# Kernel tuning notes

Measured on AMD Instinct MI355X. Metric: run time of the kernel, lower is better.

## Reference

```python
import jax, jax.numpy as jnp
import numpy as np

B, T, D, H, HD = 128, 256, 512, 8, 64

def setup_inputs() -> dict:
    key = jax.random.key(0)
    ks = jax.random.split(key, 5)
    scale = 0.02
    return {
        "x": jax.random.normal(ks[0], (B, T, D), dtype=jnp.float32),
        "Wq": jax.random.normal(ks[1], (H, D, HD), dtype=jnp.float32) * scale,
        "Wk": jax.random.normal(ks[2], (H, D, HD), dtype=jnp.float32) * scale,
        "Wv": jax.random.normal(ks[3], (H, D, HD), dtype=jnp.float32) * scale,
        "Wo": jax.random.normal(ks[4], (D, D), dtype=jnp.float32) * scale,
        "bo": jnp.zeros((D,), dtype=jnp.float32),
    }

def reference(x, Wq, Wk, Wv, Wo, bo):
    # Per-head projections, batched over heads: [B,T,D] x [H,D,HD] -> [B,H,T,HD]
    q = jnp.einsum('btd,hdk->bhtk', x, Wq)
    k = jnp.einsum('btd,hdk->bhtk', x, Wk)
    v = jnp.einsum('btd,hdk->bhtk', x, Wv)
    # Scaled scores [B,H,T,T] with causal mask
    scores = jnp.einsum('bhtk,bhsk->bhts', q, k) * (HD ** -0.5)
    causal = jnp.tril(jnp.ones((T, T), dtype=bool))
    scores = jnp.where(causal, scores, jnp.finfo(scores.dtype).min)
    attn = jax.nn.softmax(scores, axis=-1)
    # Dropout is identity at inference.
    out = jnp.einsum('bhts,bhsk->bhtk', attn, v)
    # Concat heads: [B,T,H*HD] == [B,T,D]
    out = out.transpose(0, 2, 1, 3).reshape(B, T, D)
    # Output projection
    return out @ Wo + bo
```

## Files before the change

kernel.cpp:

```cpp
#include <hip/hip_runtime.h>
#include <hip/hip_bf16.h>

typedef __bf16 bf16x8 __attribute__((ext_vector_type(8)));
typedef __bf16 bf16x4 __attribute__((ext_vector_type(4)));
typedef float f32x4 __attribute__((ext_vector_type(4)));
typedef unsigned short u16x8 __attribute__((ext_vector_type(8)));
typedef short s16x4 __attribute__((ext_vector_type(4)));


__device__ __forceinline__ unsigned short f2bf(float f) {
  unsigned u = __float_as_uint(f);
  u += 0x7fffu + ((u >> 16) & 1u);
  return (unsigned short)(u >> 16);
}

__device__ __forceinline__ bf16x4 cvt4(f32x4 v) {
  bf16x4 o;
  o[0] = (__bf16)v[0]; o[1] = (__bf16)v[1]; o[2] = (__bf16)v[2]; o[3] = (__bf16)v[3];
  return o;
}

__device__ __forceinline__ f32x4 mfma16(bf16x4 a, bf16x4 b, f32x4 c) {
#if __has_builtin(__builtin_amdgcn_mfma_f32_16x16x16_bf16)
  return __builtin_amdgcn_mfma_f32_16x16x16_bf16(a, b, c, 0, 0, 0);
#elif __has_builtin(__builtin_amdgcn_mfma_f32_16x16x16bf16_1k)
  return __builtin_amdgcn_mfma_f32_16x16x16bf16_1k(
      __builtin_bit_cast(s16x4, a), __builtin_bit_cast(s16x4, b), c, 0, 0, 0);
#else
  f32x4 d = c;
  asm("v_mfma_f32_16x16x16_bf16 %0, %1, %2, %0" : "+v"(d) : "v"(a), "v"(b));
  return d;
#endif
}

__device__ __forceinline__ void async16(const void* g, void* l) {
  __builtin_amdgcn_global_load_lds(
      (const __attribute__((address_space(1))) void*)g,
      (__attribute__((address_space(3))) void*)l, 16, 0, 0);
}

__global__ __launch_bounds__(256) void k_convert_x(const float* __restrict__ in,
                                                   unsigned short* __restrict__ out) {
  int i = blockIdx.x * 256 + threadIdx.x;
  const float4* p = (const float4*)in + (size_t)i * 2;
  float4 a = p[0], b = p[1];
  u16x8 o;
  o[0] = f2bf(a.x); o[1] = f2bf(a.y); o[2] = f2bf(a.z); o[3] = f2bf(a.w);
  o[4] = f2bf(b.x); o[5] = f2bf(b.y); o[6] = f2bf(b.z); o[7] = f2bf(b.w);
  *((u16x8*)out + i) = o;
}

__global__ __launch_bounds__(256) void k_transpose_all(const float* __restrict__ Wq,
                                                       const float* __restrict__ Wk,
                                                       const float* __restrict__ Wv,
                                                       const float* __restrict__ Wo,
                                                       unsigned short* __restrict__ Wqkv,
                                                       unsigned short* __restrict__ Wot) {
  __shared__ unsigned short tile[64][72];
  int z = blockIdx.z;
  const float* inb;
  unsigned short* outb;
  int incols, c0;
  if (z < 3) {
    const float* w = (z == 0) ? Wq : (z == 1 ? Wk : Wv);
    inb = w + (size_t)blockIdx.x * 512 * 64;
    outb = Wqkv + ((size_t)z * 8 + blockIdx.x) * 32768;
    incols = 64; c0 = 0;
  } else {
    inb = Wo; outb = Wot; incols = 512; c0 = blockIdx.x * 64;
  }
  int r0 = blockIdx.y * 64;
  int tid = threadIdx.x;
  int r = tid >> 2, cq = (tid & 3) * 16;
  const float* src = inb + (size_t)(r0 + r) * incols + c0 + cq;
#pragma unroll
  for (int i = 0; i < 16; i += 4) {
    float4 v = *(const float4*)(src + i);
    tile[r][cq + i + 0] = f2bf(v.x);
    tile[r][cq + i + 1] = f2bf(v.y);
    tile[r][cq + i + 2] = f2bf(v.z);
    tile[r][cq + i + 3] = f2bf(v.w);
  }
  __syncthreads();
  int cr = tid >> 2, rq = (tid & 3) * 16;
  u16x8 o0, o1;
#pragma unroll
  for (int i = 0; i < 8; ++i) o0[i] = tile[rq + i][cr];
#pragma unroll
  for (int i = 0; i < 8; ++i) o1[i] = tile[rq + 8 + i][cr];
  unsigned short* dst = outb + (size_t)(c0 + cr) * 512 + r0 + rq;
  *(u16x8*)dst = o0;
  *(u16x8*)(dst + 8) = o1;
}

template <bool SWAP, int EPI>
__device__ __forceinline__ void gemm_body(
    unsigned short* smem,
    const unsigned short* __restrict__ A, const unsigned short* __restrict__ Bm,
    unsigned short* __restrict__ O0, unsigned short* __restrict__ O1,
    const float* __restrict__ bo, float* __restrict__ outf,
    int m0, int n0, int mt, bool qscale) {
  int tid = threadIdx.x, wid = tid >> 6, lane = tid & 63, lr = lane & 15, lg = lane >> 4;
  int wm = wid >> 2, wn = wid & 3;
  int arow = tid >> 2;
  int sk8 = (tid & 3) ^ ((tid >> 3) & 3);
  const unsigned short* asrc = A + (size_t)(m0 + arow) * 512 + sk8 * 8;
  const unsigned short* bsrc0 = Bm + (size_t)(n0 + arow) * 512 + sk8 * 8;
  const unsigned short* bsrc1 = Bm + (size_t)(n0 + 128 + arow) * 512 + sk8 * 8;
  int rdsw = (lg ^ ((lr >> 1) & 3)) * 8;

  f32x4 acc[4][4];
#pragma unroll
  for (int mi = 0; mi < 4; ++mi)
#pragma unroll
    for (int ni = 0; ni < 4; ++ni) acc[mi][ni] = (f32x4){0.f, 0.f, 0.f, 0.f};

#define STAGE(kb, buf)                                                   \
  {                                                                      \
    unsigned short* base_ = smem + (buf) * 12288;                        \
    async16(asrc + (kb) * 32, base_ + wid * 512);                        \
    async16(bsrc0 + (kb) * 32, base_ + 4096 + wid * 512);                \
    async16(bsrc1 + (kb) * 32, base_ + 8192 + wid * 512);                \
  }

  STAGE(0, 0)
  STAGE(1, 1)
  asm volatile("s_waitcnt vmcnt(3)" ::: "memory");
  __builtin_amdgcn_s_barrier();
  asm volatile("" ::: "memory");

#pragma unroll
  for (int t = 0; t < 16; ++t) {
    int buf = t % 3;
    bf16x8 a[4], b[4];
#pragma unroll
    for (int mi = 0; mi < 4; ++mi)
      a[mi] = *(const bf16x8*)&smem[buf * 12288 + (wm * 64 + mi * 16 + lr) * 32 + rdsw];
#pragma unroll
    for (int ni = 0; ni < 4; ++ni)
      b[ni] = *(const bf16x8*)&smem[buf * 12288 + 4096 + (wn * 64 + ni * 16 + lr) * 32 + rdsw];
    if (t < 14) STAGE(t + 2, (t + 2) % 3)
    asm volatile("" ::: "memory");
    __builtin_amdgcn_s_setprio(1);
#pragma unroll
    for (int mi = 0; mi < 4; ++mi)
#pragma unroll
      for (int ni = 0; ni < 4; ++ni) {
        if (SWAP)
          acc[mi][ni] = __builtin_amdgcn_mfma_f32_16x16x32_bf16(b[ni], a[mi], acc[mi][ni], 0, 0, 0);
        else
          acc[mi][ni] = __builtin_amdgcn_mfma_f32_16x16x32_bf16(a[mi], b[ni], acc[mi][ni], 0, 0, 0);
      }
    __builtin_amdgcn_s_setprio(0);
    if (t < 14)       asm volatile("s_waitcnt vmcnt(3)" ::: "memory");
    else if (t == 14) asm volatile("s_waitcnt vmcnt(0)" ::: "memory");
    __builtin_amdgcn_s_barrier();
    asm volatile("" ::: "memory");
  }
#undef STAGE

  int bb = mt >> 1, t0 = (mt & 1) * 128;
  if constexpr (EPI == 0) {
    if (qscale) {
#pragma unroll
      for (int mi = 0; mi < 4; ++mi)
#pragma unroll
        for (int ni = 0; ni < 4; ++ni) acc[mi][ni] *= 0.18033688011112042f;
    }
    int z = n0 >> 9;
    int h = ((n0 & 511) >> 6) + wn;
    unsigned short* outp = (z ? O1 : O0) + (size_t)(bb * 8 + h) * 16384;
#pragma unroll
    for (int ni = 0; ni < 4; ++ni) {
      int hd0 = ni * 16 + lg * 4;
#pragma unroll
      for (int mi = 0; mi < 4; ++mi) {
        int tq = t0 + wm * 64 + mi * 16 + lr;
        *(bf16x4*)&outp[(size_t)tq * 64 + hd0] = cvt4(acc[mi][ni]);
      }
    }
  } else if constexpr (EPI == 1) {
#pragma unroll
    for (int ni = 0; ni < 4; ++ni) {
      int nb = n0 + wn * 64 + ni * 16 + lg * 4;
      float4 b4 = *(const float4*)&bo[nb];
#pragma unroll
      for (int mi = 0; mi < 4; ++mi) {
        int mg = m0 + wm * 64 + mi * 16 + lr;
        float4 o;
        o.x = acc[mi][ni][0] + b4.x; o.y = acc[mi][ni][1] + b4.y;
        o.z = acc[mi][ni][2] + b4.z; o.w = acc[mi][ni][3] + b4.w;
        *(float4*)&outf[(size_t)mg * 512 + nb] = o;
      }
    }
  } else {
    int h = ((n0 & 511) >> 6) + wn;
    unsigned short* outp = O0 + (size_t)(bb * 8 + h) * 16384;
#pragma unroll
    for (int ni = 0; ni < 4; ++ni) {
      int hd = ni * 16 + lr;
#pragma unroll
      for (int mi = 0; mi < 4; ++mi) {
        int tq = t0 + wm * 64 + mi * 16 + lg * 4;
        *(bf16x4*)&outp[(size_t)hd * 256 + tq] = cvt4(acc[mi][ni]);
      }
    }
  }
}

__global__ __launch_bounds__(512, 4) void k_qkv3(
    const unsigned short* __restrict__ xb,
    const unsigned short* __restrict__ Wt,
    unsigned short* __restrict__ Qb,
    unsigned short* __restrict__ Kb,
    unsigned short* __restrict__ Vtb) {
  __shared__ unsigned short smem[36864];
  int xcd = blockIdx.x & 7, g = blockIdx.x >> 3;
  int w = xcd * 192 + g;
  int mt = w / 6, nt = w % 6;
  int m0 = mt * 128, n0 = nt * 256;
  if ((n0 >> 9) < 2)
    gemm_body<true, 0>(smem, xb, Wt, Qb, Kb, nullptr, nullptr, m0, n0, mt, n0 < 512);
  else
    gemm_body<false, 2>(smem, xb, Wt, Vtb, nullptr, nullptr, nullptr, m0, n0, mt, false);
}

__global__ __launch_bounds__(512, 4) void k_oproj(
    const unsigned short* __restrict__ Ab,
    const unsigned short* __restrict__ Wot,
    const float* __restrict__ bo,
    float* __restrict__ outf) {
  __shared__ unsigned short smem[36864];
  int xcd = blockIdx.x & 7, g = blockIdx.x >> 3;
  int w = xcd * 64 + g;
  int mt = w >> 1, nt = w & 1;
  gemm_body<true, 1>(smem, Ab, Wot, nullptr, nullptr, bo, outf, mt * 128, nt * 256, mt, false);
}

__global__ __launch_bounds__(512, 4) void k_attn2(
    const unsigned short* __restrict__ Qb,
    const unsigned short* __restrict__ Kb,
    const unsigned short* __restrict__ Vtb,
    unsigned short* __restrict__ Ob) {
  __shared__ unsigned short Ksh[256 * 72];
  __shared__ unsigned short Vsh[64 * 260];
  int bh = blockIdx.x;
  int tid = threadIdx.x, wid = tid >> 6, lane = tid & 63, lr = lane & 15, lg = lane >> 4;
  int bb = bh >> 3, h = bh & 7;
  const unsigned short* Kg = Kb + (size_t)bh * 16384;
  const unsigned short* Vg = Vtb + (size_t)bh * 16384;
  int4 gk[4], gv[4];
#pragma unroll
  for (int j = 0; j < 4; ++j) {
    int c = tid + j * 512;
    gk[j] = *(const int4*)(Kg + c * 8);
    gv[j] = *(const int4*)(Vg + c * 8);
  }
  int ci0 = wid, ci1 = 15 - wid;
  const unsigned short* q0 = Qb + (size_t)bh * 16384 + (size_t)(ci0 * 16 + lr) * 64 + lg * 8;
  const unsigned short* q1 = Qb + (size_t)bh * 16384 + (size_t)(ci1 * 16 + lr) * 64 + lg * 8;
  bf16x8 bq0a = *(const bf16x8*)q0;
  bf16x8 bq0b = *(const bf16x8*)(q0 + 32);
  bf16x8 bq1a = *(const bf16x8*)q1;
  bf16x8 bq1b = *(const bf16x8*)(q1 + 32);
#pragma unroll
  for (int j = 0; j < 4; ++j) {
    int c = tid + j * 512;
    *(int4*)&Ksh[(c >> 3) * 72 + (c & 7) * 8] = gk[j];
    *(int4*)&Vsh[(c >> 5) * 260 + (c & 31) * 8] = gv[j];
  }
  __syncthreads();

  auto do_chunk = [&](int ci, bf16x8 bqa, bf16x8 bqb) {
    int t0 = ci * 16, trow = t0 + lr;
    int ntV = ci + 1;
    f32x4 acc[16];
#pragma unroll
    for (int nt = 0; nt < 16; ++nt)
      if (nt < ntV) {
        acc[nt] = (f32x4){0.f, 0.f, 0.f, 0.f};
        bf16x8 ak0 = *(const bf16x8*)&Ksh[(nt * 16 + lr) * 72 + lg * 8];
        acc[nt] = __builtin_amdgcn_mfma_f32_16x16x32_bf16(ak0, bqa, acc[nt], 0, 0, 0);
        bf16x8 ak1 = *(const bf16x8*)&Ksh[(nt * 16 + lr) * 72 + 32 + lg * 8];
        acc[nt] = __builtin_amdgcn_mfma_f32_16x16x32_bf16(ak1, bqb, acc[nt], 0, 0, 0);
      }
    float m0c = -3.0e38f, m1c = -3.0e38f;
#pragma unroll
    for (int nt = 0; nt < 16; ++nt)
      if (nt < ntV) {
        if (nt == ci) {
#pragma unroll
          for (int r = 0; r < 4; ++r) {
            float v = acc[nt][r];
            if (lg * 4 + r > lr) v = -1.0e30f;
            acc[nt][r] = v;
          }
        }
        m0c = fmaxf(m0c, fmaxf(acc[nt][0], acc[nt][1]));
        m1c = fmaxf(m1c, fmaxf(acc[nt][2], acc[nt][3]));
      }
    float m = fmaxf(m0c, m1c);
    m = fmaxf(m, __shfl_xor(m, 16));
    m = fmaxf(m, __shfl_xor(m, 32));
    float s4[4] = {0.f, 0.f, 0.f, 0.f};
    bf16x4 pk[16];
#pragma unroll
    for (int nt = 0; nt < 16; ++nt)
      if (nt < ntV) {
#pragma unroll
        for (int r = 0; r < 4; ++r) {
          float p = exp2f(acc[nt][r] - m);
          s4[r] += p;
          pk[nt][r] = (__bf16)p;
        }
      }
    float s = (s4[0] + s4[1]) + (s4[2] + s4[3]);
    s += __shfl_xor(s, 16);
    s += __shfl_xor(s, 32);
    float inv = 1.0f / s;
    f32x4 aco[4];
#pragma unroll
    for (int vt = 0; vt < 4; ++vt) aco[vt] = (f32x4){0.f, 0.f, 0.f, 0.f};
#pragma unroll
    for (int nt = 0; nt < 16; ++nt)
      if (nt < ntV) {
#pragma unroll
        for (int vt = 0; vt < 4; ++vt) {
          bf16x4 av = *(const bf16x4*)&Vsh[(vt * 16 + lr) * 260 + nt * 16 + lg * 4];
          aco[vt] = mfma16(av, pk[nt], aco[vt]);
        }
      }
    unsigned short* obase = Ob + (size_t)(bb * 256 + trow) * 512 + h * 64 + lg * 4;
#pragma unroll
    for (int vt = 0; vt < 4; ++vt) {
      bf16x4 ov;
#pragma unroll
      for (int r = 0; r < 4; ++r) ov[r] = (__bf16)(aco[vt][r] * inv);
      *(bf16x4*)(obase + vt * 16) = ov;
    }
  };

  do_chunk(ci0, bq0a, bq0b);
  do_chunk(ci1, bq1a, bq1b);
}

extern "C" void kernel_launch(void* const* d_in, const int* in_sizes, int n_in,
                              void* d_out, int out_size, void* d_ws, size_t ws_size,
                              hipStream_t stream) {
  (void)in_sizes; (void)n_in; (void)out_size; (void)ws_size;
  const float* x = (const float*)d_in[0];
  const float* Wq = (const float*)d_in[1];
  const float* Wk = (const float*)d_in[2];
  const float* Wv = (const float*)d_in[3];
  const float* Wo = (const float*)d_in[4];
  const float* bo = (const float*)d_in[5];
  float* out = (float*)d_out;
  char* ws = (char*)d_ws;
  const size_t MB = 1024 * 1024;
  unsigned short* Qb = (unsigned short*)(ws);
  unsigned short* Kb = (unsigned short*)(ws + 32 * MB);
  unsigned short* Vtb = (unsigned short*)(ws + 64 * MB);
  unsigned short* xb = (unsigned short*)(ws + 96 * MB);
  unsigned short* Wqkv = (unsigned short*)(ws + 128 * MB);
  unsigned short* Wot = Wqkv + 786432;

  hipLaunchKernelGGL(k_convert_x, dim3(8192), dim3(256), 0, stream, x, xb);
  hipLaunchKernelGGL(k_transpose_all, dim3(8, 8, 4), dim3(256), 0, stream,
                     Wq, Wk, Wv, Wo, Wqkv, Wot);
  hipLaunchKernelGGL(k_qkv3, dim3(1536), dim3(512), 0, stream, xb, Wqkv, Qb, Kb, Vtb);
  hipLaunchKernelGGL(k_attn2, dim3(1024), dim3(512), 0, stream, Qb, Kb, Vtb, xb);
  hipLaunchKernelGGL(k_oproj, dim3(512), dim3(512), 0, stream, xb, Wot, bo, out);
}
```

Before: 161.3 us.

## Replace pipelined 128x256 GEMMs with single-buffered 128x128 BK64 GEMM kernels

Replaces the 512-thread, triple-buffered 128x256 GEMM (BK=32) with a 256-thread 128x128 tile kernel that loads BK=64 chunks into a single LDS buffer, using an XOR swizzle and occupancy hint 3. The QKV projection is split into a Q/K launch and a separate V launch, and the output projection uses the same kernel. The x conversion kernel becomes grid-stride with a quarter of the blocks. This trades away overlap between global loads and MFMA (each K step now waits fully on vmcnt(0) with two barriers) in exchange for smaller tiles, more blocks per CU and less LDS per block.

```diff
diff --git a/kernel.cpp b/kernel.cpp
--- a/kernel.cpp
+++ b/kernel.cpp
@@ -41,13 +41,14 @@
 
 __global__ __launch_bounds__(256) void k_convert_x(const float* __restrict__ in,
                                                    unsigned short* __restrict__ out) {
-  int i = blockIdx.x * 256 + threadIdx.x;
-  const float4* p = (const float4*)in + (size_t)i * 2;
-  float4 a = p[0], b = p[1];
-  u16x8 o;
-  o[0] = f2bf(a.x); o[1] = f2bf(a.y); o[2] = f2bf(a.z); o[3] = f2bf(a.w);
-  o[4] = f2bf(b.x); o[5] = f2bf(b.y); o[6] = f2bf(b.z); o[7] = f2bf(b.w);
-  *((u16x8*)out + i) = o;
+  for (int i = blockIdx.x * 256 + threadIdx.x; i < 2097152; i += 2048 * 256) {
+    const float4* p = (const float4*)in + (size_t)i * 2;
+    float4 a = p[0], b = p[1];
+    u16x8 o;
+    o[0] = f2bf(a.x); o[1] = f2bf(a.y); o[2] = f2bf(a.z); o[3] = f2bf(a.w);
+    o[4] = f2bf(b.x); o[5] = f2bf(b.y); o[6] = f2bf(b.z); o[7] = f2bf(b.w);
+    *((u16x8*)out + i) = o;
+  }
 }
 
 __global__ __launch_bounds__(256) void k_transpose_all(const float* __restrict__ Wq,
@@ -93,21 +94,49 @@
   *(u16x8*)(dst + 8) = o1;
 }
 
-template <bool SWAP, int EPI>
-__device__ __forceinline__ void gemm_body(
-    unsigned short* smem,
-    const unsigned short* __restrict__ A, const unsigned short* __restrict__ Bm,
-    unsigned short* __restrict__ O0, unsigned short* __restrict__ O1,
-    const float* __restrict__ bo, float* __restrict__ outf,
-    int m0, int n0, int mt, bool qscale) {
-  int tid = threadIdx.x, wid = tid >> 6, lane = tid & 63, lr = lane & 15, lg = lane >> 4;
-  int wm = wid >> 2, wn = wid & 3;
-  int arow = tid >> 2;
-  int sk8 = (tid & 3) ^ ((tid >> 3) & 3);
-  const unsigned short* asrc = A + (size_t)(m0 + arow) * 512 + sk8 * 8;
-  const unsigned short* bsrc0 = Bm + (size_t)(n0 + arow) * 512 + sk8 * 8;
-  const unsigned short* bsrc1 = Bm + (size_t)(n0 + 128 + arow) * 512 + sk8 * 8;
-  int rdsw = (lg ^ ((lr >> 1) & 3)) * 8;
+template <int KIND>
+__global__ __launch_bounds__(256, 3) void k_gemmP(
+    const unsigned short* __restrict__ A,
+    const unsigned short* __restrict__ Bmat,
+    unsigned short* __restrict__ O0,
+    unsigned short* __restrict__ O1,
+    const float* __restrict__ bo,
+    float* __restrict__ outf) {
+  __shared__ unsigned short smem[16384];
+  const int P = (KIND == 0) ? 256 : 128;
+  int xcd = blockIdx.x & 7, g = blockIdx.x >> 3;
+  int w = xcd * P + g;
+  int mt, nt;
+  if (KIND == 0) { mt = w >> 3; nt = w & 7; }
+  else           { mt = w >> 2; nt = w & 3; }
+  int m0 = mt * 128, n0 = nt * 128;
+  int tid = threadIdx.x;
+  int wid = tid >> 6, lane = tid & 63;
+  int lr = lane & 15, lg = lane >> 4;
+  int wm = wid >> 1, wn = wid & 1;
+
+  int rowbase = wid * 32 + (lane >> 3);
+  int schunk = (lane & 7) ^ (lane >> 3);
+  auto stage = [&](int kb) {
+#pragma unroll
+    for (int j = 0; j < 4; ++j) {
+      int row = rowbase + j * 8;
+      async16(A + (size_t)(m0 + row) * 512 + kb * 64 + schunk * 8,
+              smem + (wid * 4 + j) * 512);
+      async16(Bmat + (size_t)(n0 + row) * 512 + kb * 64 + schunk * 8,
+              smem + 8192 + (wid * 4 + j) * 512);
+    }
+  };
+  auto lda = [&](int mi, int k32) -> bf16x8 {
+    int row = wm * 64 + mi * 16 + lr;
+    int ch = (k32 * 4 + lg) ^ (lr & 7);
+    return *(const bf16x8*)&smem[row * 64 + ch * 8];
+  };
+  auto ldb = [&](int ni, int k32) -> bf16x8 {
+    int row = wn * 64 + ni * 16 + lr;
+    int ch = (k32 * 4 + lg) ^ (lr & 7);
+    return *(const bf16x8*)&smem[8192 + row * 64 + ch * 8];
+  };
 
   f32x4 acc[4][4];
 #pragma unroll
@@ -115,59 +144,53 @@
 #pragma unroll
     for (int ni = 0; ni < 4; ++ni) acc[mi][ni] = (f32x4){0.f, 0.f, 0.f, 0.f};
 
-#define STAGE(kb, buf)                                                   \
-  {                                                                      \
-    unsigned short* base_ = smem + (buf) * 12288;                        \
-    async16(asrc + (kb) * 32, base_ + wid * 512);                        \
-    async16(bsrc0 + (kb) * 32, base_ + 4096 + wid * 512);                \
-    async16(bsrc1 + (kb) * 32, base_ + 8192 + wid * 512);                \
-  }
-
-  STAGE(0, 0)
-  STAGE(1, 1)
-  asm volatile("s_waitcnt vmcnt(3)" ::: "memory");
+#define MF(dst, afrag, bfrag)                                                        \
+  if constexpr (KIND == 2)                                                           \
+    dst = __builtin_amdgcn_mfma_f32_16x16x32_bf16(afrag, bfrag, dst, 0, 0, 0);       \
+  else                                                                               \
+    dst = __builtin_amdgcn_mfma_f32_16x16x32_bf16(bfrag, afrag, dst, 0, 0, 0);
+
+  stage(0);
+  asm volatile("s_waitcnt vmcnt(0)" ::: "memory");
   __builtin_amdgcn_s_barrier();
   asm volatile("" ::: "memory");
 
 #pragma unroll
-  for (int t = 0; t < 16; ++t) {
-    int buf = t % 3;
-    bf16x8 a[4], b[4];
+  for (int kb = 0; kb < 8; ++kb) {
+    bf16x8 a[4][2], b[4][2];
+#pragma unroll
+    for (int i = 0; i < 4; ++i) {
+      a[i][0] = lda(i, 0); a[i][1] = lda(i, 1);
+      b[i][0] = ldb(i, 0); b[i][1] = ldb(i, 1);
+    }
+    __builtin_amdgcn_s_setprio(1);
 #pragma unroll
     for (int mi = 0; mi < 4; ++mi)
-      a[mi] = *(const bf16x8*)&smem[buf * 12288 + (wm * 64 + mi * 16 + lr) * 32 + rdsw];
-#pragma unroll
-    for (int ni = 0; ni < 4; ++ni)
-      b[ni] = *(const bf16x8*)&smem[buf * 12288 + 4096 + (wn * 64 + ni * 16 + lr) * 32 + rdsw];
-    if (t < 14) STAGE(t + 2, (t + 2) % 3)
-    asm volatile("" ::: "memory");
-    __builtin_amdgcn_s_setprio(1);
-#pragma unroll
-    for (int mi = 0; mi < 4; ++mi)
-#pragma unroll
-      for (int ni = 0; ni < 4; ++ni) {
-        if (SWAP)
-          acc[mi][ni] = __builtin_amdgcn_mfma_f32_16x16x32_bf16(b[ni], a[mi], acc[mi][ni], 0, 0, 0);
-        else
-          acc[mi][ni] = __builtin_amdgcn_mfma_f32_16x16x32_bf16(a[mi], b[ni], acc[mi][ni], 0, 0, 0);
-      }
+#pragma unroll
+      for (int ni = 0; ni < 4; ++ni)
+#pragma unroll
+        for (int k = 0; k < 2; ++k) { MF(acc[mi][ni], a[mi][k], b[ni][k]); }
     __builtin_amdgcn_s_setprio(0);
-    if (t < 14)       asm volatile("s_waitcnt vmcnt(3)" ::: "memory");
-    else if (t == 14) asm volatile("s_waitcnt vmcnt(0)" ::: "memory");
-    __builtin_amdgcn_s_barrier();
-    asm volatile("" ::: "memory");
-  }
-#undef STAGE
+    if (kb < 7) {
+      __builtin_amdgcn_s_barrier();
+      asm volatile("" ::: "memory");
+      stage(kb + 1);
+      asm volatile("s_waitcnt vmcnt(0)" ::: "memory");
+      __builtin_amdgcn_s_barrier();
+      asm volatile("" ::: "memory");
+    }
+  }
+#undef MF
 
   int bb = mt >> 1, t0 = (mt & 1) * 128;
-  if constexpr (EPI == 0) {
-    if (qscale) {
+  if constexpr (KIND == 0) {
+    int z = n0 >> 9;
+    if (z == 0) {
 #pragma unroll
       for (int mi = 0; mi < 4; ++mi)
 #pragma unroll
         for (int ni = 0; ni < 4; ++ni) acc[mi][ni] *= 0.18033688011112042f;
     }
-    int z = n0 >> 9;
     int h = ((n0 & 511) >> 6) + wn;
     unsigned short* outp = (z ? O1 : O0) + (size_t)(bb * 8 + h) * 16384;
 #pragma unroll
@@ -179,7 +202,7 @@
         *(bf16x4*)&outp[(size_t)tq * 64 + hd0] = cvt4(acc[mi][ni]);
       }
     }
-  } else if constexpr (EPI == 1) {
+  } else if constexpr (KIND == 1) {
 #pragma unroll
     for (int ni = 0; ni < 4; ++ni) {
       int nb = n0 + wn * 64 + ni * 16 + lg * 4;
@@ -194,7 +217,7 @@
       }
     }
   } else {
-    int h = ((n0 & 511) >> 6) + wn;
+    int h = (n0 >> 6) + wn;
     unsigned short* outp = O0 + (size_t)(bb * 8 + h) * 16384;
 #pragma unroll
     for (int ni = 0; ni < 4; ++ni) {
@@ -206,35 +229,6 @@
       }
     }
   }
-}
-
-__global__ __launch_bounds__(512, 4) void k_qkv3(
-    const unsigned short* __restrict__ xb,
-    const unsigned short* __restrict__ Wt,
-    unsigned short* __restrict__ Qb,
-    unsigned short* __restrict__ Kb,
-    unsigned short* __restrict__ Vtb) {
-  __shared__ unsigned short smem[36864];
-  int xcd = blockIdx.x & 7, g = blockIdx.x >> 3;
-  int w = xcd * 192 + g;
-  int mt = w / 6, nt = w % 6;
-  int m0 = mt * 128, n0 = nt * 256;
-  if ((n0 >> 9) < 2)
-    gemm_body<true, 0>(smem, xb, Wt, Qb, Kb, nullptr, nullptr, m0, n0, mt, n0 < 512);
-  else
-    gemm_body<false, 2>(smem, xb, Wt, Vtb, nullptr, nullptr, nullptr, m0, n0, mt, false);
-}
-
-__global__ __launch_bounds__(512, 4) void k_oproj(
-    const unsigned short* __restrict__ Ab,
-    const unsigned short* __restrict__ Wot,
-    const float* __restrict__ bo,
-    float* __restrict__ outf) {
-  __shared__ unsigned short smem[36864];
-  int xcd = blockIdx.x & 7, g = blockIdx.x >> 3;
-  int w = xcd * 64 + g;
-  int mt = w >> 1, nt = w & 1;
-  gemm_body<true, 1>(smem, Ab, Wot, nullptr, nullptr, bo, outf, mt * 128, nt * 256, mt, false);
 }
 
 __global__ __launch_bounds__(512, 4) void k_attn2(
@@ -364,10 +358,16 @@
   unsigned short* Wqkv = (unsigned short*)(ws + 128 * MB);
   unsigned short* Wot = Wqkv + 786432;
 
-  hipLaunchKernelGGL(k_convert_x, dim3(8192), dim3(256), 0, stream, x, xb);
+  hipLaunchKernelGGL(k_convert_x, dim3(2048), dim3(256), 0, stream, x, xb);
   hipLaunchKernelGGL(k_transpose_all, dim3(8, 8, 4), dim3(256), 0, stream,
                      Wq, Wk, Wv, Wo, Wqkv, Wot);
-  hipLaunchKernelGGL(k_qkv3, dim3(1536), dim3(512), 0, stream, xb, Wqkv, Qb, Kb, Vtb);
+  hipLaunchKernelGGL((k_gemmP<0>), dim3(2048), dim3(256), 0, stream,
+                     xb, Wqkv, Qb, Kb, (const float*)nullptr, (float*)nullptr);
+  hipLaunchKernelGGL((k_gemmP<2>), dim3(1024), dim3(256), 0, stream,
+                     xb, Wqkv + 524288, Vtb, (unsigned short*)nullptr,
+                     (const float*)nullptr, (float*)nullptr);
   hipLaunchKernelGGL(k_attn2, dim3(1024), dim3(512), 0, stream, Qb, Kb, Vtb, xb);
-  hipLaunchKernelGGL(k_oproj, dim3(512), dim3(512), 0, stream, xb, Wot, bo, out);
-}
+  hipLaunchKernelGGL((k_gemmP<1>), dim3(1024), dim3(256), 0, stream,
+                     xb, Wqkv + 786432, (unsigned short*)nullptr, (unsigned short*)nullptr,
+                     bo, out);
+}
```

New measurement: 165.7 us. 2.8% more time.
